# Kernel optimization log

Hardware: AMD Instinct MI355X
Metric: run time of the kernel (lower is better)

## Reference

```python
import jax, jax.numpy as jnp
import numpy as np

S, A = 8, 2
SA = S + A
N = 256


def setup_inputs() -> dict:
    key = jax.random.key(0)
    ks = jax.random.split(key, 8)
    mean_full = jax.random.normal(ks[0], (SA,), dtype=jnp.float32)
    C = jax.random.normal(ks[1], (SA, SA), dtype=jnp.float32)
    cov_full = (C @ C.T) / SA + 0.1 * jnp.eye(SA, dtype=jnp.float32)  # PSD input covariance
    dynamics_inputs = jax.random.normal(ks[2], (N, SA), dtype=jnp.float32)
    dynamics_outputs = jax.random.normal(ks[3], (N, S), dtype=jnp.float32)
    eq_coeff = 0.5 + 0.5 * jax.random.uniform(ks[4], (S,), dtype=jnp.float32)
    eq_scales = 0.5 + 0.5 * jax.random.uniform(ks[5], (S, SA), dtype=jnp.float32)
    eq_noise_coeff = 1e-2 + 1e-2 * jax.random.uniform(ks[6], (S,), dtype=jnp.float32)
    return {
        'mean_full': mean_full,
        'cov_full': cov_full,
        'dynamics_inputs': dynamics_inputs,
        'dynamics_outputs': dynamics_outputs,
        'eq_coeff': eq_coeff,
        'eq_scales': eq_scales,
        'eq_noise_coeff': eq_noise_coeff,
    }


def _eq_kernel_log(x, x_, eq_coeff, eq_scales):
    # x: [n, d], x_: [m, d] -> [S, n, m] log kernel
    diffs = x[:, None, :] - x_[None, :, :]
    quads = jnp.einsum('nmd,nmd,gd->gnm', diffs, diffs, 1.0 / eq_scales)
    return jnp.log(eq_coeff)[:, None, None] - 0.5 * quads


def reference(mean_full, cov_full, dynamics_inputs, dynamics_outputs,
              eq_coeff, eq_scales, eq_noise_coeff):
    s_dim = eq_coeff.shape[0]
    sa = mean_full.shape[0]
    n = dynamics_inputs.shape[0]
    dtype = mean_full.dtype
    mean_full = mean_full.reshape(1, sa)
    cov_full = cov_full.reshape(sa, sa)
    inv_scales = 1.0 / eq_scales  # [S, SA]
    eye_sa = jnp.eye(sa, dtype=dtype)

    # data covariance K + noise: [S, N, N]
    log_K = _eq_kernel_log(dynamics_inputs, dynamics_inputs, eq_coeff, eq_scales)
    data_cov = jnp.exp(log_K) + eq_noise_coeff[:, None, None] * eye_sa[None, :n, :n] if n == sa else jnp.exp(log_K) + eq_noise_coeff[:, None, None] * jnp.eye(n, dtype=dtype)[None]
    # beta: [S, N]
    beta = jnp.linalg.solve(data_cov, dynamics_outputs.T[:, :, None])[:, :, 0]

    # mean determinant coefficient: det(cov_full diag(1/scales_g) + I)^(-1/2)
    M = cov_full[None, :, :] * inv_scales[:, None, :] + eye_sa[None]  # [S, SA, SA]
    mean_det_coeff = eq_coeff * jnp.linalg.det(M) ** (-0.5)  # [S]

    cov_full_plus_scales = cov_full[None] + jax.vmap(jnp.diag)(eq_scales)  # [S, SA, SA]
    nu = dynamics_inputs - mean_full  # [N, SA]
    sol = jnp.linalg.solve(cov_full_plus_scales,
                           jnp.broadcast_to(nu.T[None], (s_dim, sa, n)))  # [S, SA, N]
    mean_quad = jnp.einsum('id,gdi->gi', nu, sol)
    mean_exp_quad = mean_det_coeff[:, None] * jnp.exp(-0.5 * mean_quad)  # [S, N]
    mean = jnp.einsum('gi,gi->g', beta, mean_exp_quad)  # [S]

    # R_ab = cov_full (inv_a + inv_b) + I: [S, S, SA, SA]
    cross = inv_scales[:, None, :] + inv_scales[None, :, :]  # [S, S, SA]
    R = cov_full[None, None, :, :] * cross[:, :, None, :] + eye_sa[None, None]
    _, log_R_det = jnp.linalg.slogdet(R)
    log_R_det_inv_sqrt = -0.5 * log_R_det  # [S, S]

    log_k_data_mu = _eq_kernel_log(mean_full, dynamics_inputs, eq_coeff, eq_scales)  # [S, 1, N]
    log_k_ab = log_k_data_mu[None, :, :, :] + log_k_data_mu[:, :, :, None]  # [S, S, N, N]

    eq_scale_times_nu = nu[None, :, :] * inv_scales[:, None, :]  # [S, N, SA]
    z = (eq_scale_times_nu[:, None, :, None, :] +
         eq_scale_times_nu[None, :, None, :, :])  # [S, S, N, N, SA]
    # R^{-1} cov_full, then quadratic form z^T (R^{-1} cov_full) z
    R_inv = jnp.linalg.inv(R)  # [S, S, SA, SA]
    M_ab = jnp.einsum('abij,jk->abik', R_inv, cov_full)  # [S, S, SA, SA]
    cov_quad = 0.5 * jnp.einsum('abnmi,abij,abnmj->abnm', z, M_ab, z)

    log_Q = log_k_ab + cov_quad + log_R_det_inv_sqrt[:, :, None, None]
    Q = jnp.exp(log_Q)  # [S, S, N, N]

    Q_diag = Q[jnp.arange(s_dim), jnp.arange(s_dim)]  # [S, N, N]
    expected_var = eq_coeff - jnp.trace(jnp.linalg.solve(data_cov, Q_diag),
                                        axis1=-2, axis2=-1)  # [S]

    cov = jnp.einsum('ai,bj,abij->ab', beta, beta, Q)
    cov = cov - mean[:, None] * mean[None, :]
    cov = cov + jnp.diag(expected_var)

    # input-output cross covariance
    A_inv_mean = jnp.linalg.solve(cov_full_plus_scales,
                                  jnp.broadcast_to(mean_full.T[None], (s_dim, sa, 1)))  # [S, SA, 1]
    A_inv_dyn = jnp.linalg.solve(cov_full_plus_scales,
                                 jnp.broadcast_to(dynamics_inputs.T[None], (s_dim, sa, n)))  # [S, SA, N]
    cross_cov_mu = eq_scales[:, :, None] * A_inv_mean + jnp.einsum('ij,gjk->gik', cov_full, A_inv_dyn)
    cross_cov = jnp.einsum('gk,gdk,gk->dg', mean_exp_quad, cross_cov_mu, beta)  # [SA, S]
    cross_cov_s = cross_cov[:s_dim, :] - mean_full[:, :s_dim].T * mean[None, :]

    mean = mean + mean_full[0, :s_dim]
    cov = cov + cov_full[:s_dim, :s_dim]
    cov = cov + cross_cov_s + cross_cov_s.T
    return mean, cov
```

## Files before the change

### kernel.cpp

```cpp
#include <hip/hip_runtime.h>
#include <math.h>

#define S_DIM 8
#define SA_DIM 10
#define NN 256

constexpr size_t OFF_K     = 0;
constexpr size_t OFF_LINV  = OFF_K    + 8ull*NN*NN;
constexpr size_t OFF_KINV  = OFF_LINV + 8ull*NN*NN;
constexpr size_t OFF_RD    = OFF_KINV + 8ull*NN*NN;
constexpr size_t OFF_U     = OFF_RD   + 8*NN;
constexpr size_t OFF_LK    = OFF_U    + 8*NN*SA_DIM;
constexpr size_t OFF_M     = OFF_LK   + 8*NN;
constexpr size_t OFF_C     = OFF_M    + 64*100;
constexpr size_t OFF_AINV  = OFF_C    + 64;
constexpr size_t OFF_AIM   = OFF_AINV + 800;
constexpr size_t OFF_MDC   = OFF_AIM  + 80;
constexpr size_t OFF_MEAN  = OFF_MDC  + 8;
constexpr size_t OFF_CROSS = OFF_MEAN + 8;
constexpr size_t OFF_COVP  = OFF_CROSS+ 80;
constexpr size_t OFF_TRP   = OFF_COVP + 256;

__device__ void gj_invert10(float A[SA_DIM][SA_DIM], float B[SA_DIM][SA_DIM], float* logdet) {
#pragma unroll
  for (int i = 0; i < SA_DIM; i++)
#pragma unroll
    for (int j = 0; j < SA_DIM; j++) B[i][j] = (i == j) ? 1.f : 0.f;
  float ld = 0.f;
#pragma unroll
  for (int k = 0; k < SA_DIM; k++) {
    float pv = A[k][k];
    ld += logf(pv);
    float ip = 1.f / pv;
#pragma unroll
    for (int j = 0; j < SA_DIM; j++) { A[k][j] *= ip; B[k][j] *= ip; }
#pragma unroll
    for (int r = 0; r < SA_DIM; r++) {
      if (r == k) continue;
      float f = A[r][k];
#pragma unroll
      for (int j = 0; j < SA_DIM; j++) { A[r][j] -= f * A[k][j]; B[r][j] -= f * B[k][j]; }
    }
  }
  *logdet = ld;
}

__global__ __launch_bounds__(256) void k_front(const float* __restrict__ x,
                                               const float* __restrict__ mf,
                                               const float* __restrict__ cov,
                                               const float* __restrict__ eqc,
                                               const float* __restrict__ scales,
                                               const float* __restrict__ noise,
                                               float* __restrict__ Kw,
                                               float* __restrict__ u,
                                               float* __restrict__ lkw,
                                               float* __restrict__ Mw, float* __restrict__ cvec,
                                               float* __restrict__ Ainvw, float* __restrict__ aimw,
                                               float* __restrict__ mdcw) {
  int blk = blockIdx.x;
  if (blk < 2048) {
    int g = blk >> 8;
    int n = blk & 255;
    int m = threadIdx.x;
    __shared__ float xs[NN * SA_DIM];
    __shared__ float isc[SA_DIM];
    for (int i = threadIdx.x; i < NN * SA_DIM; i += 256) xs[i] = x[i];
    if (threadIdx.x < SA_DIM) isc[threadIdx.x] = 1.0f / scales[g * SA_DIM + threadIdx.x];
    __syncthreads();
    float quad = 0.f;
#pragma unroll
    for (int d = 0; d < SA_DIM; d++) {
      float df = xs[n * SA_DIM + d] - xs[m * SA_DIM + d];
      quad += df * df * isc[d];
    }
    float v = eqc[g] * __expf(-0.5f * quad);
    if (m == n) v += noise[g];
    Kw[(size_t)g * NN * NN + (size_t)n * NN + m] = v;
  } else if (blk < 2056) {
    int g = blk - 2048;
    int n = threadIdx.x;
    float quad = 0.f;
#pragma unroll
    for (int d = 0; d < SA_DIM; d++) {
      float isc = 1.0f / scales[g * SA_DIM + d];
      float nu = x[n * SA_DIM + d] - mf[d];
      u[((size_t)g * NN + n) * SA_DIM + d] = nu * isc;
      quad += nu * nu * isc;
    }
    lkw[g * NN + n] = logf(eqc[g]) - 0.5f * quad;
  } else {
    int p = threadIdx.x;
    if (p >= 64) return;
    int a = p >> 3, b = p & 7;
    float A[SA_DIM][SA_DIM], B[SA_DIM][SA_DIM];
    for (int i = 0; i < SA_DIM; i++)
      for (int j = 0; j < SA_DIM; j++)
        A[i][j] = cov[i * SA_DIM + j] * (1.f / scales[a * SA_DIM + j] + 1.f / scales[b * SA_DIM + j]) +
                  ((i == j) ? 1.f : 0.f);
    float ld;
    gj_invert10(A, B, &ld);
    cvec[p] = -0.5f * ld;
    for (int i = 0; i < SA_DIM; i++)
      for (int j = 0; j < SA_DIM; j++) {
        float v = 0.f;
        for (int k = 0; k < SA_DIM; k++) v += B[i][k] * cov[k * SA_DIM + j];
        Mw[p * 100 + i * SA_DIM + j] = v;
      }
    if (b == 0) {
      int g = a;
      for (int i = 0; i < SA_DIM; i++)
        for (int j = 0; j < SA_DIM; j++)
          A[i][j] = cov[i * SA_DIM + j] + ((i == j) ? scales[g * SA_DIM + j] : 0.f);
      float ld2;
      gj_invert10(A, B, &ld2);
      for (int i = 0; i < SA_DIM; i++)
        for (int j = 0; j < SA_DIM; j++) Ainvw[g * 100 + i * SA_DIM + j] = B[i][j];
      for (int i = 0; i < SA_DIM; i++) {
        float v = 0.f;
        for (int j = 0; j < SA_DIM; j++) v += B[i][j] * mf[j];
        aimw[g * SA_DIM + i] = v;
      }
      for (int i = 0; i < SA_DIM; i++)
        for (int j = 0; j < SA_DIM; j++)
          A[i][j] = cov[i * SA_DIM + j] * (1.f / scales[g * SA_DIM + j]) + ((i == j) ? 1.f : 0.f);
      float ld3;
      gj_invert10(A, B, &ld3);
      mdcw[g] = eqc[g] * __expf(-0.5f * ld3);
    }
  }
}

__global__ __launch_bounds__(1024) void k_chol6(float* __restrict__ Aw, float* __restrict__ rd) {
  int g = blockIdx.x;
  float* Ag = Aw + (size_t)g * NN * NN;
  float* rdg = rd + g * NN;
  int t = threadIdx.x;
  int lane = t & 63;
  int w = t >> 6;
  __shared__ __align__(16) float P[16][248];

  for (int p = 0; p < 16; p++) {
    int c0 = 16 * p;
    int nb = NN - c0 - 16;
    if (w < 4) {
      int rr = lane & 15;
      float a[16];
      float myrs = 0.f;
#pragma unroll
      for (int j = 0; j < 16; j++)
        a[j] = (j <= rr) ? Ag[(size_t)(c0 + j) * NN + (c0 + rr)]
                         : Ag[(size_t)(c0 + rr) * NN + (c0 + j)];
#pragma unroll
      for (int k = 0; k < 16; k++) {
        float d = __shfl(a[k], k);
        float rs_ = rsqrtf(d);
        if (rr == k) myrs = rs_;
        float m = a[k] * rs_;
#pragma unroll
        for (int j = 0; j < 16; j++) {
          if (j > k) {
            float Lkj = __shfl(a[j], k) * rs_;
            a[j] = fmaf(-m, Lkj, a[j]);
          }
        }
        a[k] = m;
      }
      if (w == 0 && lane < 16) {
        rdg[c0 + rr] = myrs;
#pragma unroll
        for (int j = 0; j < 16; j++)
          if (j <= rr) Ag[(size_t)(c0 + j) * NN + (c0 + rr)] = a[j];
      }
      if (t < nb) {
        int i = c0 + 16 + t;
        float xs[16];
#pragma unroll
        for (int c = 0; c < 16; c++) {
          float x = Ag[(size_t)(c0 + c) * NN + i];
#pragma unroll
          for (int cp = 0; cp < 16; cp++) {
            if (cp < c) {
              float Lccp = __shfl(a[cp], c);
              x = fmaf(-Lccp, xs[cp], x);
            }
          }
          xs[c] = x * __shfl(myrs, c);
        }
#pragma unroll
        for (int c = 0; c < 16; c++) {
          Ag[(size_t)(c0 + c) * NN + i] = xs[c];
          P[c][t] = xs[c];
        }
      }
    }
    __syncthreads();
    if (nb > 0) {
      int nt4 = nb >> 2;
      int ntile = nt4 * (nt4 + 1) / 2;
      for (int tau = t; tau < ntile; tau += 1024) {
        int rt = ntile - 1 - tau;
        int q = (int)((sqrtf((float)(8 * rt + 1)) - 1.0f) * 0.5f);
        while ((q + 1) * (q + 2) / 2 <= rt) q++;
        while (q * (q + 1) / 2 > rt) q--;
        int jq = nt4 - 1 - q;
        int rem = rt - q * (q + 1) / 2;
        int iq = nt4 - 1 - rem;
        int jb = c0 + 16 + 4 * jq;
        int ib = c0 + 16 + 4 * iq;
        float4 cv0 = *(const float4*)(Ag + (size_t)(jb + 0) * NN + ib);
        float4 cv1 = *(const float4*)(Ag + (size_t)(jb + 1) * NN + ib);
        float4 cv2 = *(const float4*)(Ag + (size_t)(jb + 2) * NN + ib);
        float4 cv3 = *(const float4*)(Ag + (size_t)(jb + 3) * NN + ib);
        float4 a0 = make_float4(0.f, 0.f, 0.f, 0.f);
        float4 a1 = a0, a2 = a0, a3 = a0;
#pragma unroll
        for (int k = 0; k < 16; k++) {
          float4 pi = *(const float4*)(&P[k][4 * iq]);
          float4 pj = *(const float4*)(&P[k][4 * jq]);
          a0.x = fmaf(pj.x, pi.x, a0.x); a0.y = fmaf(pj.x, pi.y, a0.y);
          a0.z = fmaf(pj.x, pi.z, a0.z); a0.w = fmaf(pj.x, pi.w, a0.w);
          a1.x = fmaf(pj.y, pi.x, a1.x); a1.y = fmaf(pj.y, pi.y, a1.y);
          a1.z = fmaf(pj.y, pi.z, a1.z); a1.w = fmaf(pj.y, pi.w, a1.w);
          a2.x = fmaf(pj.z, pi.x, a2.x); a2.y = fmaf(pj.z, pi.y, a2.y);
          a2.z = fmaf(pj.z, pi.z, a2.z); a2.w = fmaf(pj.z, pi.w, a2.w);
          a3.x = fmaf(pj.w, pi.x, a3.x); a3.y = fmaf(pj.w, pi.y, a3.y);
          a3.z = fmaf(pj.w, pi.z, a3.z); a3.w = fmaf(pj.w, pi.w, a3.w);
        }
        cv0.x -= a0.x; cv0.y -= a0.y; cv0.z -= a0.z; cv0.w -= a0.w;
        cv1.x -= a1.x; cv1.y -= a1.y; cv1.z -= a1.z; cv1.w -= a1.w;
        cv2.x -= a2.x; cv2.y -= a2.y; cv2.z -= a2.z; cv2.w -= a2.w;
        cv3.x -= a3.x; cv3.y -= a3.y; cv3.z -= a3.z; cv3.w -= a3.w;
        *(float4*)(Ag + (size_t)(jb + 0) * NN + ib) = cv0;
        *(float4*)(Ag + (size_t)(jb + 1) * NN + ib) = cv1;
        *(float4*)(Ag + (size_t)(jb + 2) * NN + ib) = cv2;
        *(float4*)(Ag + (size_t)(jb + 3) * NN + ib) = cv3;
      }
    }
    __syncthreads();
  }
}

__global__ __launch_bounds__(256) void k_linv2(const float* __restrict__ LT,
                                               const float* __restrict__ rd,
                                               float* __restrict__ Linv) {
  int g = blockIdx.x >> 2;
  int q = blockIdx.x & 3;
  int w = threadIdx.x >> 6;
  int lane = threadIdx.x & 63;
  int j = 4 * q + w;
  const float* Ag = LT + (size_t)g * NN * NN;
  const float* rdg = rd + g * NN;
  float* Og = Linv + (size_t)g * NN * NN;
  __shared__ __align__(16) float Xl[4][16][16][16];
  __shared__ __align__(16) float Dv[16][16][16];
  int r = lane & 15, cq = lane >> 4;

  for (int s = 0; s < 4; s++) {
    int i = w + 4 * s;
    for (int e = lane; e < 256; e += 64) {
      int k = e >> 4, rr = e & 15;
      Xl[w][s][k][rr] = Ag[(size_t)(16 * i + k) * NN + 16 * i + rr];
    }
    asm volatile("s_waitcnt lgkmcnt(0)" ::: "memory");
    __builtin_amdgcn_sched_barrier(0);
    int c = lane & 15;
    float x0, x1, x2, x3, x4, x5, x6, x7, x8, x9, x10, x11, x12, x13, x14, x15;
    float xv[16];
#pragma unroll
    for (int rr = 0; rr < 16; rr++) {
      float tmp = (rr == c) ? 1.f : 0.f;
#pragma unroll
      for (int m = 0; m < 16; m++) {
        if (m < rr) tmp = fmaf(-Xl[w][s][m][rr], xv[m], tmp);
      }
      xv[rr] = tmp * rdg[16 * i + rr];
    }
    (void)x0;(void)x1;(void)x2;(void)x3;(void)x4;(void)x5;(void)x6;(void)x7;
    (void)x8;(void)x9;(void)x10;(void)x11;(void)x12;(void)x13;(void)x14;(void)x15;
    if (lane < 16) {
#pragma unroll
      for (int rr = 0; rr < 16; rr++) Dv[i][rr][lane] = xv[rr];
    }
  }
  __syncthreads();

  {
    float4 dj = *(const float4*)&Dv[j][r][4 * cq];
    *(float4*)&Xl[w][j][r][4 * cq] = dj;
    *(float4*)(Og + (size_t)(16 * j + r) * NN + 16 * j + 4 * cq) = dj;
    float4 z = make_float4(0.f, 0.f, 0.f, 0.f);
    for (int i2 = 0; i2 < j; i2++)
      *(float4*)(Og + (size_t)(16 * i2 + r) * NN + 16 * j + 4 * cq) = z;
  }
  asm volatile("s_waitcnt lgkmcnt(0)" ::: "memory");
  __builtin_amdgcn_sched_barrier(0);

  for (int i = j + 1; i < 16; i++) {
    float4 acc = make_float4(0.f, 0.f, 0.f, 0.f);
    for (int k = j; k < i; k++) {
      const float* Lbase = Ag + (size_t)(16 * k) * NN + 16 * i + r;
      const float* Xk = &Xl[w][k][0][4 * cq];
#pragma unroll
      for (int m = 0; m < 16; m++) {
        float lv = Lbase[(size_t)m * NN];
        float4 xvv = *(const float4*)(Xk + 16 * m);
        acc.x = fmaf(lv, xvv.x, acc.x);
        acc.y = fmaf(lv, xvv.y, acc.y);
        acc.z = fmaf(lv, xvv.z, acc.z);
        acc.w = fmaf(lv, xvv.w, acc.w);
      }
    }
    float4 o = make_float4(0.f, 0.f, 0.f, 0.f);
#pragma unroll
    for (int m = 0; m < 16; m++) {
      float d = Dv[i][r][m];
      float sx = __shfl(acc.x, m + 16 * cq);
      float sy = __shfl(acc.y, m + 16 * cq);
      float sz = __shfl(acc.z, m + 16 * cq);
      float sw = __shfl(acc.w, m + 16 * cq);
      o.x = fmaf(-d, sx, o.x);
      o.y = fmaf(-d, sy, o.y);
      o.z = fmaf(-d, sz, o.z);
      o.w = fmaf(-d, sw, o.w);
    }
    *(float4*)&Xl[w][i][r][4 * cq] = o;
    *(float4*)(Og + (size_t)(16 * i + r) * NN + 16 * j + 4 * cq) = o;
    asm volatile("s_waitcnt lgkmcnt(0)" ::: "memory");
    __builtin_amdgcn_sched_barrier(0);
  }
}

__global__ __launch_bounds__(256) void k_syrk(const float* __restrict__ Linv,
                                              float* __restrict__ Kinv) {
  int g = blockIdx.x >> 4;
  int tile = blockIdx.x & 15;
  int i0 = (tile >> 2) * 64, j0 = (tile & 3) * 64;
  const float* A = Linv + (size_t)g * NN * NN;
  float* O = Kinv + (size_t)g * NN * NN;
  __shared__ float sa[32][64], sb[32][64];
  int tx = threadIdx.x & 15, ty = threadIdx.x >> 4;
  float acc[4][4] = {{0.f}};
  for (int k0 = 0; k0 < NN; k0 += 32) {
    for (int e = threadIdx.x; e < 2048; e += 256) {
      int kk = e >> 6, cc = e & 63;
      sa[kk][cc] = A[(size_t)(k0 + kk) * NN + i0 + cc];
      sb[kk][cc] = A[(size_t)(k0 + kk) * NN + j0 + cc];
    }
    __syncthreads();
#pragma unroll 8
    for (int kk = 0; kk < 32; kk++) {
      float av[4], bv[4];
#pragma unroll
      for (int q = 0; q < 4; q++) { av[q] = sa[kk][ty * 4 + q]; bv[q] = sb[kk][tx * 4 + q]; }
#pragma unroll
      for (int q = 0; q < 4; q++)
#pragma unroll
        for (int r = 0; r < 4; r++) acc[q][r] += av[q] * bv[r];
    }
    __syncthreads();
  }
#pragma unroll
  for (int q = 0; q < 4; q++)
#pragma unroll
    for (int r = 0; r < 4; r++)
      O[(size_t)(i0 + ty * 4 + q) * NN + j0 + tx * 4 + r] = acc[q][r];
}

__global__ __launch_bounds__(256) void k_back(const float* __restrict__ u,
                                              const float* __restrict__ lkw,
                                              const float* __restrict__ Mw,
                                              const float* __restrict__ cvec,
                                              const float* __restrict__ Kinv,
                                              const float* __restrict__ y,
                                              const float* __restrict__ x,
                                              const float* __restrict__ mf,
                                              const float* __restrict__ cov,
                                              const float* __restrict__ scales,
                                              const float* __restrict__ Ainvw,
                                              const float* __restrict__ aimw,
                                              const float* __restrict__ mdcw,
                                              float* __restrict__ covp, float* __restrict__ trp,
                                              float* __restrict__ meanw, float* __restrict__ crossw) {
  int blk = blockIdx.x;
  int t = threadIdx.x;
  if (blk < 256) {
    int p = blk >> 2;
    int quarter = blk & 3;
    int a = p >> 3, b = p & 7;
    __shared__ __align__(16) float ub[NN * SA_DIM];
    __shared__ float Ms[100];
    __shared__ float sbv[NN];
    __shared__ __align__(16) float eb[NN];
    __shared__ __align__(16) float ysb[NN];
    __shared__ __align__(16) float ysa[NN];
    __shared__ float red[256];
    for (int idx = t; idx < NN * SA_DIM; idx += 256) ub[idx] = u[(size_t)b * NN * SA_DIM + idx];
    if (t < 100) Ms[t] = Mw[p * 100 + t];
    ysb[t] = y[t * S_DIM + b];
    ysa[t] = y[t * S_DIM + a];
    __syncthreads();
    {
      const float4* Kb = (const float4*)(Kinv + (size_t)b * NN * NN + (size_t)t * NN);
      float acc = 0.f;
      for (int m4 = 0; m4 < 64; m4++) {
        float4 kv = Kb[m4];
        float4 yv = ((const float4*)ysb)[m4];
        acc += kv.x * yv.x + kv.y * yv.y + kv.z * yv.z + kv.w * yv.w;
      }
      eb[t] = acc;
      int m = t;
      float qd = 0.f;
#pragma unroll
      for (int d = 0; d < SA_DIM; d++) {
        float v = 0.f;
#pragma unroll
        for (int e = 0; e < SA_DIM; e++) v += Ms[d * SA_DIM + e] * ub[m * SA_DIM + e];
        qd += v * ub[m * SA_DIM + d];
      }
      sbv[m] = lkw[b * NN + m] + 0.5f * qd;
    }
    __syncthreads();
    int n = quarter * 64 + (t >> 2);
    int c = t & 3;
    float ua[SA_DIM];
#pragma unroll
    for (int d = 0; d < SA_DIM; d++) ua[d] = u[((size_t)a * NN + n) * SA_DIM + d];
    float va[SA_DIM];
#pragma unroll
    for (int d = 0; d < SA_DIM; d++) {
      float v = 0.f;
#pragma unroll
      for (int e = 0; e < SA_DIM; e++) v += Ms[d * SA_DIM + e] * ua[e];
      va[d] = v;
    }
    float qa = 0.f;
#pragma unroll
    for (int d = 0; d < SA_DIM; d++) qa += va[d] * ua[d];
    float pa = lkw[a * NN + n] + 0.5f * qa + cvec[p];
    float wa;
    if (a == b) {
      wa = eb[n];
    } else {
      const float4* Ka = (const float4*)(Kinv + (size_t)a * NN * NN + (size_t)n * NN);
      float acc = 0.f;
      for (int m4 = 0; m4 < 64; m4++) {
        float4 kv = Ka[m4];
        float4 yv = ((const float4*)ysa)[m4];
        acc += kv.x * yv.x + kv.y * yv.y + kv.z * yv.z + kv.w * yv.w;
      }
      wa = acc;
    }
    const float* Krow = Kinv + (size_t)a * NN * NN + (size_t)n * NN;
    float covacc = 0.f, tracc = 0.f;
    bool dg = (a == b);
    for (int ii = 0; ii < 64; ii++) {
      int mm = c + 4 * ii;
      float s = pa + sbv[mm];
#pragma unroll
      for (int d = 0; d < SA_DIM; d++) s += va[d] * ub[mm * SA_DIM + d];
      float e = __expf(s);
      covacc += eb[mm] * e;
      if (dg) tracc += Krow[mm] * e;
    }
    covacc *= wa;
    red[t] = covacc;
    __syncthreads();
    for (int st = 128; st > 0; st >>= 1) {
      if (t < st) red[t] += red[t + st];
      __syncthreads();
    }
    if (t == 0) covp[blk] = red[0];
    if (dg) {
      red[t] = tracc;
      __syncthreads();
      for (int st = 128; st > 0; st >>= 1) {
        if (t < st) red[t] += red[t + st];
        __syncthreads();
      }
      if (t == 0) trp[a * 4 + quarter] = red[0];
    }
  } else {
    int g = blk - 256;
    int i = t;
    __shared__ float Ai[100], cv[100], aims[SA_DIM], sc[SA_DIM], mfs[SA_DIM];
    __shared__ __align__(16) float ys[NN];
    __shared__ float red[256];
    if (i < 100) { Ai[i] = Ainvw[g * 100 + i]; cv[i] = cov[i]; }
    if (i < SA_DIM) { aims[i] = aimw[g * SA_DIM + i]; sc[i] = scales[g * SA_DIM + i]; mfs[i] = mf[i]; }
    ys[i] = y[i * S_DIM + g];
    __syncthreads();
    float bg;
    {
      const float4* Kg = (const float4*)(Kinv + (size_t)g * NN * NN + (size_t)i * NN);
      float acc = 0.f;
      for (int m4 = 0; m4 < 64; m4++) {
        float4 kv = Kg[m4];
        float4 yv = ((const float4*)ys)[m4];
        acc += kv.x * yv.x + kv.y * yv.y + kv.z * yv.z + kv.w * yv.w;
      }
      bg = acc;
    }
    float xi[SA_DIM], nu[SA_DIM];
#pragma unroll
    for (int d = 0; d < SA_DIM; d++) { xi[d] = x[i * SA_DIM + d]; nu[d] = xi[d] - mfs[d]; }
    float sv[SA_DIM], ad[SA_DIM];
#pragma unroll
    for (int d = 0; d < SA_DIM; d++) {
      float s1 = 0.f, s2 = 0.f;
#pragma unroll
      for (int e = 0; e < SA_DIM; e++) { s1 += Ai[d * SA_DIM + e] * nu[e]; s2 += Ai[d * SA_DIM + e] * xi[e]; }
      sv[d] = s1;
      ad[d] = s2;
    }
    float mq = 0.f;
#pragma unroll
    for (int d = 0; d < SA_DIM; d++) mq += nu[d] * sv[d];
    float mexp = mdcw[g] * __expf(-0.5f * mq);
    float cm = bg * mexp;
    float contrib[SA_DIM];
#pragma unroll
    for (int d = 0; d < SA_DIM; d++) {
      float ccm = sc[d] * aims[d];
#pragma unroll
      for (int jj = 0; jj < SA_DIM; jj++) ccm += cv[d * SA_DIM + jj] * ad[jj];
      contrib[d] = mexp * ccm * bg;
    }
    red[i] = cm;
    __syncthreads();
    for (int st = 128; st > 0; st >>= 1) {
      if (i < st) red[i] += red[i + st];
      __syncthreads();
    }
    if (i == 0) meanw[g] = red[0];
    for (int d = 0; d < SA_DIM; d++) {
      __syncthreads();
      red[i] = contrib[d];
      __syncthreads();
      for (int st = 128; st > 0; st >>= 1) {
        if (i < st) red[i] += red[i + st];
        __syncthreads();
      }
      if (i == 0) crossw[d * S_DIM + g] = red[0];
    }
  }
}

__global__ __launch_bounds__(64) void k_final(const float* __restrict__ covp,
                                              const float* __restrict__ trp,
                                              const float* __restrict__ meanw,
                                              const float* __restrict__ crossw,
                                              const float* __restrict__ cov,
                                              const float* __restrict__ eqc,
                                              const float* __restrict__ mf,
                                              float* __restrict__ out) {
  int p = threadIdx.x;
  if (p >= 64) return;
  int a = p >> 3, b = p & 7;
  float covq = covp[p * 4] + covp[p * 4 + 1] + covp[p * 4 + 2] + covp[p * 4 + 3];
  float ma = meanw[a], mb = meanw[b];
  float val = covq - ma * mb + cov[a * SA_DIM + b];
  if (a == b) {
    float tr = trp[a * 4] + trp[a * 4 + 1] + trp[a * 4 + 2] + trp[a * 4 + 3];
    val += eqc[a] - tr;
  }
  val += (crossw[a * S_DIM + b] - mf[a] * mb) + (crossw[b * S_DIM + a] - mf[b] * ma);
  out[S_DIM + p] = val;
  if (p < S_DIM) out[p] = meanw[p] + mf[p];
}

extern "C" void kernel_launch(void* const* d_in, const int* in_sizes, int n_in,
                              void* d_out, int out_size, void* d_ws, size_t ws_size,
                              hipStream_t stream) {
  const float* mf     = (const float*)d_in[0];
  const float* cov    = (const float*)d_in[1];
  const float* x      = (const float*)d_in[2];
  const float* y      = (const float*)d_in[3];
  const float* eqc    = (const float*)d_in[4];
  const float* scales = (const float*)d_in[5];
  const float* noise  = (const float*)d_in[6];
  float* ws = (float*)d_ws;

  float* Kw    = ws + OFF_K;
  float* Linv  = ws + OFF_LINV;
  float* Kinv  = ws + OFF_KINV;
  float* rd    = ws + OFF_RD;
  float* u     = ws + OFF_U;
  float* lkw   = ws + OFF_LK;
  float* Mw    = ws + OFF_M;
  float* cvec  = ws + OFF_C;
  float* Ainvw = ws + OFF_AINV;
  float* aimw  = ws + OFF_AIM;
  float* mdcw  = ws + OFF_MDC;
  float* meanw = ws + OFF_MEAN;
  float* crossw= ws + OFF_CROSS;
  float* covp  = ws + OFF_COVP;
  float* trp   = ws + OFF_TRP;

  k_front<<<2057, 256, 0, stream>>>(x, mf, cov, eqc, scales, noise, Kw, u, lkw, Mw, cvec,
                                    Ainvw, aimw, mdcw);
  k_chol6<<<8, 1024, 0, stream>>>(Kw, rd);
  k_linv2<<<32, 256, 0, stream>>>(Kw, rd, Linv);
  k_syrk<<<128, 256, 0, stream>>>(Linv, Kinv);
  k_back<<<264, 256, 0, stream>>>(u, lkw, Mw, cvec, Kinv, y, x, mf, cov, scales,
                                  Ainvw, aimw, mdcw, covp, trp, meanw, crossw);
  k_final<<<1, 64, 0, stream>>>(covp, trp, meanw, crossw, cov, eqc, mf, (float*)d_out);
}
```

Baseline: 304.1 us.

## Stage next Cholesky panel in LDS, hoist beta into its own kernel, pad u rows

The Cholesky update loop now handles at most two tiles per thread, loading both C tiles before computing. It also writes the next 16-row panel into a shared NP buffer so the following step reads it from LDS instead of global memory. Beta = Kinv·y is computed once per output dimension in a new k_beta kernel, replacing the repeated matvecs inside k_back's 264 blocks. The u rows in LDS are padded to 12 floats so they can be read as float4, at the cost of one extra launch and more shared memory in the Cholesky kernel.

```diff
diff --git a/kernel.cpp b/kernel.cpp
--- a/kernel.cpp
+++ b/kernel.cpp
@@ -16,7 +16,8 @@
 constexpr size_t OFF_AINV  = OFF_C    + 64;
 constexpr size_t OFF_AIM   = OFF_AINV + 800;
 constexpr size_t OFF_MDC   = OFF_AIM  + 80;
-constexpr size_t OFF_MEAN  = OFF_MDC  + 8;
+constexpr size_t OFF_BETA  = OFF_MDC  + 8;
+constexpr size_t OFF_MEAN  = OFF_BETA + 8*NN;
 constexpr size_t OFF_CROSS = OFF_MEAN + 8;
 constexpr size_t OFF_COVP  = OFF_CROSS+ 80;
 constexpr size_t OFF_TRP   = OFF_COVP + 256;
@@ -130,7 +131,20 @@
   }
 }
 
-__global__ __launch_bounds__(1024) void k_chol6(float* __restrict__ Aw, float* __restrict__ rd) {
+__device__ __forceinline__ void tile_idx(int tau, int ntile, int nt4, int c0,
+                                         int& ib, int& jb, int& iq, int& jq) {
+  int rt = ntile - 1 - tau;
+  int q = (int)((sqrtf((float)(8 * rt + 1)) - 1.0f) * 0.5f);
+  while ((q + 1) * (q + 2) / 2 <= rt) q++;
+  while (q * (q + 1) / 2 > rt) q--;
+  jq = nt4 - 1 - q;
+  int rem = rt - q * (q + 1) / 2;
+  iq = nt4 - 1 - rem;
+  jb = c0 + 16 + 4 * jq;
+  ib = c0 + 16 + 4 * iq;
+}
+
+__global__ __launch_bounds__(1024) void k_chol7(float* __restrict__ Aw, float* __restrict__ rd) {
   int g = blockIdx.x;
   float* Ag = Aw + (size_t)g * NN * NN;
   float* rdg = rd + g * NN;
@@ -138,6 +152,7 @@
   int lane = t & 63;
   int w = t >> 6;
   __shared__ __align__(16) float P[16][248];
+  __shared__ __align__(16) float NP[16][248];
 
   for (int p = 0; p < 16; p++) {
     int c0 = 16 * p;
@@ -146,10 +161,16 @@
       int rr = lane & 15;
       float a[16];
       float myrs = 0.f;
-#pragma unroll
-      for (int j = 0; j < 16; j++)
-        a[j] = (j <= rr) ? Ag[(size_t)(c0 + j) * NN + (c0 + rr)]
-                         : Ag[(size_t)(c0 + rr) * NN + (c0 + j)];
+      if (p == 0) {
+#pragma unroll
+        for (int j = 0; j < 16; j++)
+          a[j] = (j <= rr) ? Ag[(size_t)(c0 + j) * NN + (c0 + rr)]
+                           : Ag[(size_t)(c0 + rr) * NN + (c0 + j)];
+      } else {
+#pragma unroll
+        for (int j = 0; j < 16; j++)
+          a[j] = (j <= rr) ? NP[j][rr] : NP[rr][j];
+      }
 #pragma unroll
       for (int k = 0; k < 16; k++) {
         float d = __shfl(a[k], k);
@@ -176,7 +197,7 @@
         float xs[16];
 #pragma unroll
         for (int c = 0; c < 16; c++) {
-          float x = Ag[(size_t)(c0 + c) * NN + i];
+          float x = (p == 0) ? Ag[(size_t)(c0 + c) * NN + i] : NP[c][16 + t];
 #pragma unroll
           for (int cp = 0; cp < 16; cp++) {
             if (cp < c) {
@@ -197,44 +218,58 @@
     if (nb > 0) {
       int nt4 = nb >> 2;
       int ntile = nt4 * (nt4 + 1) / 2;
-      for (int tau = t; tau < ntile; tau += 1024) {
-        int rt = ntile - 1 - tau;
-        int q = (int)((sqrtf((float)(8 * rt + 1)) - 1.0f) * 0.5f);
-        while ((q + 1) * (q + 2) / 2 <= rt) q++;
-        while (q * (q + 1) / 2 > rt) q--;
-        int jq = nt4 - 1 - q;
-        int rem = rt - q * (q + 1) / 2;
-        int iq = nt4 - 1 - rem;
-        int jb = c0 + 16 + 4 * jq;
-        int ib = c0 + 16 + 4 * iq;
-        float4 cv0 = *(const float4*)(Ag + (size_t)(jb + 0) * NN + ib);
-        float4 cv1 = *(const float4*)(Ag + (size_t)(jb + 1) * NN + ib);
-        float4 cv2 = *(const float4*)(Ag + (size_t)(jb + 2) * NN + ib);
-        float4 cv3 = *(const float4*)(Ag + (size_t)(jb + 3) * NN + ib);
-        float4 a0 = make_float4(0.f, 0.f, 0.f, 0.f);
-        float4 a1 = a0, a2 = a0, a3 = a0;
-#pragma unroll
-        for (int k = 0; k < 16; k++) {
-          float4 pi = *(const float4*)(&P[k][4 * iq]);
-          float4 pj = *(const float4*)(&P[k][4 * jq]);
-          a0.x = fmaf(pj.x, pi.x, a0.x); a0.y = fmaf(pj.x, pi.y, a0.y);
-          a0.z = fmaf(pj.x, pi.z, a0.z); a0.w = fmaf(pj.x, pi.w, a0.w);
-          a1.x = fmaf(pj.y, pi.x, a1.x); a1.y = fmaf(pj.y, pi.y, a1.y);
-          a1.z = fmaf(pj.y, pi.z, a1.z); a1.w = fmaf(pj.y, pi.w, a1.w);
-          a2.x = fmaf(pj.z, pi.x, a2.x); a2.y = fmaf(pj.z, pi.y, a2.y);
-          a2.z = fmaf(pj.z, pi.z, a2.z); a2.w = fmaf(pj.z, pi.w, a2.w);
-          a3.x = fmaf(pj.w, pi.x, a3.x); a3.y = fmaf(pj.w, pi.y, a3.y);
-          a3.z = fmaf(pj.w, pi.z, a3.z); a3.w = fmaf(pj.w, pi.w, a3.w);
-        }
-        cv0.x -= a0.x; cv0.y -= a0.y; cv0.z -= a0.z; cv0.w -= a0.w;
-        cv1.x -= a1.x; cv1.y -= a1.y; cv1.z -= a1.z; cv1.w -= a1.w;
-        cv2.x -= a2.x; cv2.y -= a2.y; cv2.z -= a2.z; cv2.w -= a2.w;
-        cv3.x -= a3.x; cv3.y -= a3.y; cv3.z -= a3.z; cv3.w -= a3.w;
-        *(float4*)(Ag + (size_t)(jb + 0) * NN + ib) = cv0;
-        *(float4*)(Ag + (size_t)(jb + 1) * NN + ib) = cv1;
-        *(float4*)(Ag + (size_t)(jb + 2) * NN + ib) = cv2;
-        *(float4*)(Ag + (size_t)(jb + 3) * NN + ib) = cv3;
-      }
+      int tau0 = t, tau1 = t + 1024;
+      bool h0 = tau0 < ntile, h1 = tau1 < ntile;
+      int ib0 = 0, jb0 = 0, iq0 = 0, jq0 = 0, ib1 = 0, jb1 = 0, iq1 = 0, jq1 = 0;
+      float4 A0, A1, A2, A3, B0, B1, B2, B3;
+      if (h0) {
+        tile_idx(tau0, ntile, nt4, c0, ib0, jb0, iq0, jq0);
+        A0 = *(const float4*)(Ag + (size_t)(jb0 + 0) * NN + ib0);
+        A1 = *(const float4*)(Ag + (size_t)(jb0 + 1) * NN + ib0);
+        A2 = *(const float4*)(Ag + (size_t)(jb0 + 2) * NN + ib0);
+        A3 = *(const float4*)(Ag + (size_t)(jb0 + 3) * NN + ib0);
+      }
+      if (h1) {
+        tile_idx(tau1, ntile, nt4, c0, ib1, jb1, iq1, jq1);
+        B0 = *(const float4*)(Ag + (size_t)(jb1 + 0) * NN + ib1);
+        B1 = *(const float4*)(Ag + (size_t)(jb1 + 1) * NN + ib1);
+        B2 = *(const float4*)(Ag + (size_t)(jb1 + 2) * NN + ib1);
+        B3 = *(const float4*)(Ag + (size_t)(jb1 + 3) * NN + ib1);
+      }
+#define TILE_BODY(HAS, IQ, JQ, IB, JB, C0v, C1v, C2v, C3v)                         \
+      if (HAS) {                                                                   \
+        float4 a0 = make_float4(0.f, 0.f, 0.f, 0.f), a1 = a0, a2 = a0, a3 = a0;    \
+        _Pragma("unroll")                                                          \
+        for (int k = 0; k < 16; k++) {                                             \
+          float4 pi = *(const float4*)(&P[k][4 * (IQ)]);                           \
+          float4 pj = *(const float4*)(&P[k][4 * (JQ)]);                           \
+          a0.x = fmaf(pj.x, pi.x, a0.x); a0.y = fmaf(pj.x, pi.y, a0.y);            \
+          a0.z = fmaf(pj.x, pi.z, a0.z); a0.w = fmaf(pj.x, pi.w, a0.w);            \
+          a1.x = fmaf(pj.y, pi.x, a1.x); a1.y = fmaf(pj.y, pi.y, a1.y);            \
+          a1.z = fmaf(pj.y, pi.z, a1.z); a1.w = fmaf(pj.y, pi.w, a1.w);            \
+          a2.x = fmaf(pj.z, pi.x, a2.x); a2.y = fmaf(pj.z, pi.y, a2.y);            \
+          a2.z = fmaf(pj.z, pi.z, a2.z); a2.w = fmaf(pj.z, pi.w, a2.w);            \
+          a3.x = fmaf(pj.w, pi.x, a3.x); a3.y = fmaf(pj.w, pi.y, a3.y);            \
+          a3.z = fmaf(pj.w, pi.z, a3.z); a3.w = fmaf(pj.w, pi.w, a3.w);            \
+        }                                                                          \
+        C0v.x -= a0.x; C0v.y -= a0.y; C0v.z -= a0.z; C0v.w -= a0.w;                \
+        C1v.x -= a1.x; C1v.y -= a1.y; C1v.z -= a1.z; C1v.w -= a1.w;                \
+        C2v.x -= a2.x; C2v.y -= a2.y; C2v.z -= a2.z; C2v.w -= a2.w;                \
+        C3v.x -= a3.x; C3v.y -= a3.y; C3v.z -= a3.z; C3v.w -= a3.w;                \
+        *(float4*)(Ag + (size_t)((JB) + 0) * NN + (IB)) = C0v;                     \
+        *(float4*)(Ag + (size_t)((JB) + 1) * NN + (IB)) = C1v;                     \
+        *(float4*)(Ag + (size_t)((JB) + 2) * NN + (IB)) = C2v;                     \
+        *(float4*)(Ag + (size_t)((JB) + 3) * NN + (IB)) = C3v;                     \
+        if ((JQ) < 4) {                                                            \
+          *(float4*)(&NP[4 * (JQ) + 0][4 * (IQ)]) = C0v;                           \
+          *(float4*)(&NP[4 * (JQ) + 1][4 * (IQ)]) = C1v;                           \
+          *(float4*)(&NP[4 * (JQ) + 2][4 * (IQ)]) = C2v;                           \
+          *(float4*)(&NP[4 * (JQ) + 3][4 * (IQ)]) = C3v;                           \
+        }                                                                          \
+      }
+      TILE_BODY(h0, iq0, jq0, ib0, jb0, A0, A1, A2, A3)
+      TILE_BODY(h1, iq1, jq1, ib1, jb1, B0, B1, B2, B3)
+#undef TILE_BODY
     }
     __syncthreads();
   }
@@ -264,7 +299,6 @@
     asm volatile("s_waitcnt lgkmcnt(0)" ::: "memory");
     __builtin_amdgcn_sched_barrier(0);
     int c = lane & 15;
-    float x0, x1, x2, x3, x4, x5, x6, x7, x8, x9, x10, x11, x12, x13, x14, x15;
     float xv[16];
 #pragma unroll
     for (int rr = 0; rr < 16; rr++) {
@@ -275,8 +309,6 @@
       }
       xv[rr] = tmp * rdg[16 * i + rr];
     }
-    (void)x0;(void)x1;(void)x2;(void)x3;(void)x4;(void)x5;(void)x6;(void)x7;
-    (void)x8;(void)x9;(void)x10;(void)x11;(void)x12;(void)x13;(void)x14;(void)x15;
     if (lane < 16) {
 #pragma unroll
       for (int rr = 0; rr < 16; rr++) Dv[i][rr][lane] = xv[rr];
@@ -366,12 +398,29 @@
       O[(size_t)(i0 + ty * 4 + q) * NN + j0 + tx * 4 + r] = acc[q][r];
 }
 
+__global__ __launch_bounds__(256) void k_beta(const float* __restrict__ Kinv,
+                                              const float* __restrict__ y,
+                                              float* __restrict__ betaw) {
+  int g = blockIdx.x, n = threadIdx.x;
+  __shared__ __align__(16) float ys[NN];
+  ys[n] = y[n * S_DIM + g];
+  __syncthreads();
+  const float4* Kg = (const float4*)(Kinv + (size_t)g * NN * NN + (size_t)n * NN);
+  float acc = 0.f;
+  for (int m4 = 0; m4 < 64; m4++) {
+    float4 kv = Kg[m4];
+    float4 yv = ((const float4*)ys)[m4];
+    acc += kv.x * yv.x + kv.y * yv.y + kv.z * yv.z + kv.w * yv.w;
+  }
+  betaw[g * NN + n] = acc;
+}
+
 __global__ __launch_bounds__(256) void k_back(const float* __restrict__ u,
                                               const float* __restrict__ lkw,
                                               const float* __restrict__ Mw,
                                               const float* __restrict__ cvec,
                                               const float* __restrict__ Kinv,
-                                              const float* __restrict__ y,
+                                              const float* __restrict__ betaw,
                                               const float* __restrict__ x,
                                               const float* __restrict__ mf,
                                               const float* __restrict__ cov,
@@ -387,37 +436,31 @@
     int p = blk >> 2;
     int quarter = blk & 3;
     int a = p >> 3, b = p & 7;
-    __shared__ __align__(16) float ub[NN * SA_DIM];
+    __shared__ __align__(16) float ub[NN * 12];
     __shared__ float Ms[100];
     __shared__ float sbv[NN];
-    __shared__ __align__(16) float eb[NN];
-    __shared__ __align__(16) float ysb[NN];
-    __shared__ __align__(16) float ysa[NN];
+    __shared__ float eb[NN];
     __shared__ float red[256];
-    for (int idx = t; idx < NN * SA_DIM; idx += 256) ub[idx] = u[(size_t)b * NN * SA_DIM + idx];
+    {
+      const float* ur = u + (size_t)b * NN * SA_DIM + (size_t)t * SA_DIM;
+      float* ud = &ub[t * 12];
+#pragma unroll
+      for (int d = 0; d < SA_DIM; d++) ud[d] = ur[d];
+    }
     if (t < 100) Ms[t] = Mw[p * 100 + t];
-    ysb[t] = y[t * S_DIM + b];
-    ysa[t] = y[t * S_DIM + a];
+    eb[t] = betaw[b * NN + t];
     __syncthreads();
     {
-      const float4* Kb = (const float4*)(Kinv + (size_t)b * NN * NN + (size_t)t * NN);
-      float acc = 0.f;
-      for (int m4 = 0; m4 < 64; m4++) {
-        float4 kv = Kb[m4];
-        float4 yv = ((const float4*)ysb)[m4];
-        acc += kv.x * yv.x + kv.y * yv.y + kv.z * yv.z + kv.w * yv.w;
-      }
-      eb[t] = acc;
-      int m = t;
+      const float* um = &ub[t * 12];
       float qd = 0.f;
 #pragma unroll
       for (int d = 0; d < SA_DIM; d++) {
         float v = 0.f;
 #pragma unroll
-        for (int e = 0; e < SA_DIM; e++) v += Ms[d * SA_DIM + e] * ub[m * SA_DIM + e];
-        qd += v * ub[m * SA_DIM + d];
-      }
-      sbv[m] = lkw[b * NN + m] + 0.5f * qd;
+        for (int e = 0; e < SA_DIM; e++) v += Ms[d * SA_DIM + e] * um[e];
+        qd += v * um[d];
+      }
+      sbv[t] = lkw[b * NN + t] + 0.5f * qd;
     }
     __syncthreads();
     int n = quarter * 64 + (t >> 2);
@@ -437,27 +480,20 @@
 #pragma unroll
     for (int d = 0; d < SA_DIM; d++) qa += va[d] * ua[d];
     float pa = lkw[a * NN + n] + 0.5f * qa + cvec[p];
-    float wa;
-    if (a == b) {
-      wa = eb[n];
-    } else {
-      const float4* Ka = (const float4*)(Kinv + (size_t)a * NN * NN + (size_t)n * NN);
-      float acc = 0.f;
-      for (int m4 = 0; m4 < 64; m4++) {
-        float4 kv = Ka[m4];
-        float4 yv = ((const float4*)ysa)[m4];
-        acc += kv.x * yv.x + kv.y * yv.y + kv.z * yv.z + kv.w * yv.w;
-      }
-      wa = acc;
-    }
+    float wa = betaw[a * NN + n];
     const float* Krow = Kinv + (size_t)a * NN * NN + (size_t)n * NN;
     float covacc = 0.f, tracc = 0.f;
     bool dg = (a == b);
     for (int ii = 0; ii < 64; ii++) {
       int mm = c + 4 * ii;
+      const float* ur = &ub[mm * 12];
+      float4 f0 = *(const float4*)ur;
+      float4 f1 = *(const float4*)(ur + 4);
+      float4 f2 = *(const float4*)(ur + 8);
       float s = pa + sbv[mm];
-#pragma unroll
-      for (int d = 0; d < SA_DIM; d++) s += va[d] * ub[mm * SA_DIM + d];
+      s += va[0] * f0.x + va[1] * f0.y + va[2] * f0.z + va[3] * f0.w;
+      s += va[4] * f1.x + va[5] * f1.y + va[6] * f1.z + va[7] * f1.w;
+      s += va[8] * f2.x + va[9] * f2.y;
       float e = __expf(s);
       covacc += eb[mm] * e;
       if (dg) tracc += Krow[mm] * e;
@@ -483,23 +519,11 @@
     int g = blk - 256;
     int i = t;
     __shared__ float Ai[100], cv[100], aims[SA_DIM], sc[SA_DIM], mfs[SA_DIM];
-    __shared__ __align__(16) float ys[NN];
     __shared__ float red[256];
     if (i < 100) { Ai[i] = Ainvw[g * 100 + i]; cv[i] = cov[i]; }
     if (i < SA_DIM) { aims[i] = aimw[g * SA_DIM + i]; sc[i] = scales[g * SA_DIM + i]; mfs[i] = mf[i]; }
-    ys[i] = y[i * S_DIM + g];
-    __syncthreads();
-    float bg;
-    {
-      const float4* Kg = (const float4*)(Kinv + (size_t)g * NN * NN + (size_t)i * NN);
-      float acc = 0.f;
-      for (int m4 = 0; m4 < 64; m4++) {
-        float4 kv = Kg[m4];
-        float4 yv = ((const float4*)ys)[m4];
-        acc += kv.x * yv.x + kv.y * yv.y + kv.z * yv.z + kv.w * yv.w;
-      }
-      bg = acc;
-    }
+    __syncthreads();
+    float bg = betaw[g * NN + i];
     float xi[SA_DIM], nu[SA_DIM];
 #pragma unroll
     for (int d = 0; d < SA_DIM; d++) { xi[d] = x[i * SA_DIM + d]; nu[d] = xi[d] - mfs[d]; }
@@ -591,6 +615,7 @@
   float* Ainvw = ws + OFF_AINV;
   float* aimw  = ws + OFF_AIM;
   float* mdcw  = ws + OFF_MDC;
+  float* betaw = ws + OFF_BETA;
   float* meanw = ws + OFF_MEAN;
   float* crossw= ws + OFF_CROSS;
   float* covp  = ws + OFF_COVP;
@@ -598,10 +623,11 @@
 
   k_front<<<2057, 256, 0, stream>>>(x, mf, cov, eqc, scales, noise, Kw, u, lkw, Mw, cvec,
                                     Ainvw, aimw, mdcw);
-  k_chol6<<<8, 1024, 0, stream>>>(Kw, rd);
+  k_chol7<<<8, 1024, 0, stream>>>(Kw, rd);
   k_linv2<<<32, 256, 0, stream>>>(Kw, rd, Linv);
   k_syrk<<<128, 256, 0, stream>>>(Linv, Kinv);
-  k_back<<<264, 256, 0, stream>>>(u, lkw, Mw, cvec, Kinv, y, x, mf, cov, scales,
+  k_beta<<<8, 256, 0, stream>>>(Kinv, y, betaw);
+  k_back<<<264, 256, 0, stream>>>(u, lkw, Mw, cvec, Kinv, betaw, x, mf, cov, scales,
                                   Ainvw, aimw, mdcw, covp, trp, meanw, crossw);
   k_final<<<1, 64, 0, stream>>>(covp, trp, meanw, crossw, cov, eqc, mf, (float*)d_out);
 }
```

New measurement: 437.3 us. +43.8%, slower.
